# Optimization experiments

Hardware: AMD Instinct MI355X
Metric: run time of the kernel (lower is better)

The kernel has to match this reference:

```python
import jax, jax.numpy as jnp
import numpy as np

N_NODES = 50000
N_EDGES = 400000
IN_DIM = 128
HIDDEN = 128
OUT_DIM = 128
MIX = 4

def _gelu(x):
    return jax.nn.gelu(x, approximate=False)  # torch default erf-GELU

def setup_inputs() -> dict:
    key = jax.random.key(0)
    ks = jax.random.split(key, 8)
    X = jax.random.normal(ks[0], (N_NODES, IN_DIM), dtype=jnp.float32)
    edge_index = jax.random.randint(ks[1], (2, N_EDGES), 0, N_NODES, dtype=jnp.int64)
    s = lambda fan_in: 1.0 / np.sqrt(fan_in)
    W1 = jax.random.uniform(ks[2], (HIDDEN, IN_DIM), jnp.float32, -s(IN_DIM), s(IN_DIM))
    b1 = jax.random.uniform(ks[3], (HIDDEN,), jnp.float32, -s(IN_DIM), s(IN_DIM))
    WA = jax.random.uniform(ks[4], (HIDDEN, HIDDEN), jnp.float32, -s(HIDDEN), s(HIDDEN))
    WB = jax.random.uniform(ks[5], (MIX, HIDDEN), jnp.float32, -s(HIDDEN), s(HIDDEN))
    W2 = jax.random.uniform(ks[6], (OUT_DIM, 2 * HIDDEN), jnp.float32, -s(2 * HIDDEN), s(2 * HIDDEN))
    b2 = jax.random.uniform(ks[7], (OUT_DIM,), jnp.float32, -s(2 * HIDDEN), s(2 * HIDDEN))
    return {"X": X, "edge_index": edge_index, "W1": W1, "b1": b1,
            "WA": WA, "WB": WB, "W2": W2, "b2": b2}

def reference(X, edge_index, W1, b1, WA, WB, W2, b2):
    num_nodes = X.shape[0]
    # ff1 -> gelu (dropout identity in eval)
    H = _gelu(X @ W1.T + b1)                       # (N, h)
    src, dst = edge_index[0], edge_index[1]
    X_src = H[src]                                 # (E, h) gather
    # hyper target weights per edge
    W_tar = _gelu(X_src @ WA.T) @ WB.T             # (E, m)
    # per-edge outer product, scatter_add over dst
    cross = X_src[:, :, None] * W_tar[:, None, :]  # (E, h, m)
    agg = jax.ops.segment_sum(cross, dst, num_segments=num_nodes)  # (N, h, m)
    agg = _gelu(agg)
    # gather back per edge, contract mix dim
    out_edge = jnp.einsum('ehm,em->eh', agg[dst], W_tar)  # (E, h)
    # scatter_mean over dst
    ones = jnp.ones((src.shape[0],), X.dtype)
    cnt = jax.ops.segment_sum(ones, dst, num_segments=num_nodes)   # (N,)
    agg_node = jax.ops.segment_sum(out_edge, dst, num_segments=num_nodes)
    agg_node = agg_node / jnp.maximum(cnt, 1.0)[:, None]           # (N, h)
    # root connection + gelu, ff2
    feat = _gelu(jnp.concatenate([agg_node, H], axis=1))           # (N, 2h)
    out = feat @ W2.T + b2                                          # (N, out)
    return out
```

## Files before the change

### kernel.cpp

```cpp
#include <hip/hip_runtime.h>
#include <hip/hip_bf16.h>

#define NN 50000
#define NE 400000
#define NT 3125

typedef unsigned short u16;
typedef short short8 __attribute__((ext_vector_type(8)));
typedef float f32x4 __attribute__((ext_vector_type(4)));

__device__ __forceinline__ float geluf(float x){ return 0.5f*x*(1.0f+erff(x*0.70710678118654752440f)); }
__device__ __forceinline__ u16 f2bfb(float f){
  union { __hip_bfloat16 h; u16 u; } cv; cv.h = __float2bfloat16(f); return cv.u;
}
__device__ __forceinline__ float bfb2f(u16 u){ return __uint_as_float(((unsigned)u)<<16); }

__global__ __launch_bounds__(256) void k_pre(const float* __restrict__ W1,
    const float* __restrict__ WA, const float* __restrict__ W2,
    u16* __restrict__ W1b, u16* __restrict__ WAb, u16* __restrict__ W2b,
    const int* __restrict__ dst, int* __restrict__ deg)
{
  if (blockIdx.x < 64){
    int i4 = (blockIdx.x*256 + threadIdx.x) * 4;
    const float* srcp; u16* dstp; int off;
    if (i4 < 16384){ srcp = W1; dstp = W1b; off = i4; }
    else if (i4 < 32768){ srcp = WA; dstp = WAb; off = i4 - 16384; }
    else { srcp = W2; dstp = W2b; off = i4 - 32768; }
    float4 v = *(const float4*)(srcp + off);
    ushort4 o;
    o.x = f2bfb(v.x); o.y = f2bfb(v.y); o.z = f2bfb(v.z); o.w = f2bfb(v.w);
    *(ushort4*)(dstp + off) = o;
  } else {
    int e = (blockIdx.x - 64)*256 + threadIdx.x;
    if (e < NE) atomicAdd(&deg[dst[e]], 1);
  }
}

__global__ __launch_bounds__(512) void k_ff1n(const float* __restrict__ X,
    const u16* __restrict__ W1b, const float* __restrict__ b1,
    const u16* __restrict__ WAb, const float* __restrict__ WB,
    u16* __restrict__ Hb, float* __restrict__ T)
{
  extern __shared__ u16 smem[];
  u16* w1s = smem;
  u16* was = smem + 17408;
  const int LDW = 136;
  for (int idx8 = threadIdx.x*8; idx8 < 128*128; idx8 += 512*8){
    int c = idx8 >> 7, k = idx8 & 127;
    *(short8*)&w1s[c*LDW + k] = *(const short8*)(W1b + idx8);
    *(short8*)&was[c*LDW + k] = *(const short8*)(WAb + idx8);
  }
  __syncthreads();
  const int lane = threadIdx.x & 63;
  const int wave = threadIdx.x >> 6;
  const int lrow = lane & 15;
  const int kgrp = lane >> 4;
  u16* hls = smem + 34816 + wave*(16*LDW);
  float4 b1v[8];
  #pragma unroll
  for (int nb = 0; nb < 8; nb++) b1v[nb] = *(const float4*)(b1 + nb*16 + kgrp*4);
  float wbv[4][8];
  #pragma unroll
  for (int m = 0; m < 4; m++)
    #pragma unroll
    for (int nb = 0; nb < 8; nb++)
      wbv[m][nb] = WB[m*128 + nb*16 + lrow];
  for (int tile = blockIdx.x*8 + wave; tile < NT; tile += gridDim.x*8){
    const float* xr = X + (size_t)(tile*16 + lrow)*128 + kgrp*8;
    f32x4 acc[8];
    #pragma unroll
    for (int nb = 0; nb < 8; nb++) acc[nb] = (f32x4){0.f,0.f,0.f,0.f};
    #pragma unroll
    for (int kk = 0; kk < 4; kk++){
      float4 xa = *(const float4*)(xr + kk*32);
      float4 xb = *(const float4*)(xr + kk*32 + 4);
      union { short8 v; u16 u[8]; } af;
      af.u[0]=f2bfb(xa.x); af.u[1]=f2bfb(xa.y); af.u[2]=f2bfb(xa.z); af.u[3]=f2bfb(xa.w);
      af.u[4]=f2bfb(xb.x); af.u[5]=f2bfb(xb.y); af.u[6]=f2bfb(xb.z); af.u[7]=f2bfb(xb.w);
      #pragma unroll
      for (int nb = 0; nb < 8; nb++){
        short8 bf = *(const short8*)&w1s[(nb*16 + lrow)*LDW + kk*32 + kgrp*8];
        acc[nb] = __builtin_amdgcn_mfma_f32_16x16x32_bf16(bf, af.v, acc[nb], 0, 0, 0);
      }
    }
    const size_t rb = (size_t)(tile*16 + lrow)*128 + kgrp*4;
    #pragma unroll
    for (int nb = 0; nb < 8; nb++){
      ushort4 hp;
      #pragma unroll
      for (int r = 0; r < 4; r++)
        ((u16*)&hp)[r] = f2bfb(geluf(acc[nb][r] + b1v[nb][r]));
      *(ushort4*)(Hb + rb + nb*16) = hp;
      *(ushort4*)&hls[lrow*LDW + nb*16 + kgrp*4] = hp;
    }
    f32x4 acc2[8];
    #pragma unroll
    for (int nb = 0; nb < 8; nb++) acc2[nb] = (f32x4){0.f,0.f,0.f,0.f};
    #pragma unroll
    for (int kk = 0; kk < 4; kk++){
      short8 af = *(const short8*)&hls[lrow*LDW + kk*32 + kgrp*8];
      #pragma unroll
      for (int nb = 0; nb < 8; nb++){
        short8 bf = *(const short8*)&was[(nb*16 + lrow)*LDW + kk*32 + kgrp*8];
        acc2[nb] = __builtin_amdgcn_mfma_f32_16x16x32_bf16(af, bf, acc2[nb], 0, 0, 0);
      }
    }
    float part[4][4];
    #pragma unroll
    for (int r = 0; r < 4; r++)
      #pragma unroll
      for (int m = 0; m < 4; m++) part[r][m] = 0.f;
    #pragma unroll
    for (int nb = 0; nb < 8; nb++){
      float g0 = geluf(acc2[nb][0]), g1 = geluf(acc2[nb][1]);
      float g2 = geluf(acc2[nb][2]), g3 = geluf(acc2[nb][3]);
      #pragma unroll
      for (int m = 0; m < 4; m++){
        float w = wbv[m][nb];
        part[0][m] += g0*w; part[1][m] += g1*w;
        part[2][m] += g2*w; part[3][m] += g3*w;
      }
    }
    #pragma unroll
    for (int s = 1; s < 16; s <<= 1)
      #pragma unroll
      for (int r = 0; r < 4; r++)
        #pragma unroll
        for (int m = 0; m < 4; m++)
          part[r][m] += __shfl_xor(part[r][m], s, 64);
    if (lrow == 0){
      #pragma unroll
      for (int r = 0; r < 4; r++){
        f32x4 tv = { part[r][0], part[r][1], part[r][2], part[r][3] };
        *(f32x4*)&T[(size_t)(tile*16 + kgrp*4 + r)*4] = tv;
      }
    }
  }
}

__global__ __launch_bounds__(1024) void k_scan(const int* __restrict__ deg, int* __restrict__ offs){
  __shared__ int wsum[16];
  __shared__ int sbase_s;
  const int tid = threadIdx.x, lane = tid & 63, wave = tid >> 6;
  if (tid == 0) sbase_s = 0;
  __syncthreads();
  for (int base = 0; base < NN; base += 4096){
    int i0 = base + tid*4;
    int v0=0,v1=0,v2=0,v3=0;
    if (i0+3 < NN){ int4 v = *(const int4*)(deg+i0); v0=v.x;v1=v.y;v2=v.z;v3=v.w; }
    else {
      if (i0   < NN) v0 = deg[i0];
      if (i0+1 < NN) v1 = deg[i0+1];
      if (i0+2 < NN) v2 = deg[i0+2];
    }
    int own = v0+v1+v2+v3;
    int inc = own;
    #pragma unroll
    for (int s=1;s<64;s<<=1){ int t = __shfl_up(inc, s, 64); if (lane >= s) inc += t; }
    if (lane == 63) wsum[wave] = inc;
    __syncthreads();
    if (wave == 0 && lane < 16){
      int w = wsum[lane];
      #pragma unroll
      for (int s=1;s<16;s<<=1){ int t = __shfl_up(w, s, 64); if (lane >= s) w += t; }
      wsum[lane] = w;
    }
    __syncthreads();
    int sbase = sbase_s;
    int wbase = sbase + (wave ? wsum[wave-1] : 0);
    int excl = wbase + inc - own;
    if (i0   < NN) offs[i0]   = excl;
    if (i0+1 < NN) offs[i0+1] = excl + v0;
    if (i0+2 < NN) offs[i0+2] = excl + v0+v1;
    if (i0+3 < NN) offs[i0+3] = excl + v0+v1+v2;
    __syncthreads();
    if (tid == 0) sbase_s = sbase + wsum[15];
    __syncthreads();
  }
  if (tid == 0) offs[NN] = sbase_s;
}

__global__ void k_fill(const int* __restrict__ src, const int* __restrict__ dst,
                       const int* __restrict__ offs, int* __restrict__ cur,
                       int* __restrict__ slist){
  int e = blockIdx.x*256 + threadIdx.x;
  if (e < NE){
    int d = dst[e];
    int p = atomicAdd(&cur[d], 1);
    slist[offs[d] + p] = src[e];
  }
}

__global__ __launch_bounds__(256) void k_agg(const u16* __restrict__ Hb,
    const float* __restrict__ T, const int* __restrict__ offs,
    const int* __restrict__ slist, u16* __restrict__ GAb)
{
  const int lane = threadIdx.x & 63;
  const int wave = threadIdx.x >> 6;
  const int vo = lane*2;
  for (int v = blockIdx.x*4 + wave; v < NN; v += gridDim.x*4){
    const int e0 = __builtin_amdgcn_readfirstlane(offs[v]);
    const int e1 = __builtin_amdgcn_readfirstlane(offs[v+1]);
    float ax0=0, ax1=0, ax2=0, ax3=0;
    float ay0=0, ay1=0, ay2=0, ay3=0;
    float s0=0, s1=0, s2=0, s3=0;
    int idx = e0;
    for (; idx + 8 <= e1; idx += 8){
      unsigned pk[8]; float4 tt[8];
      #pragma unroll
      for (int u = 0; u < 8; u++){
        int sn = slist[idx+u];
        pk[u] = *(const unsigned*)(Hb + (size_t)sn*128 + vo);
        tt[u] = *(const float4*)(T + (size_t)sn*4);
      }
      #pragma unroll
      for (int u = 0; u < 8; u++){
        float hx = bfb2f((u16)(pk[u] & 0xffffu));
        float hy = bfb2f((u16)(pk[u] >> 16));
        ax0 += hx*tt[u].x; ax1 += hx*tt[u].y; ax2 += hx*tt[u].z; ax3 += hx*tt[u].w;
        ay0 += hy*tt[u].x; ay1 += hy*tt[u].y; ay2 += hy*tt[u].z; ay3 += hy*tt[u].w;
        s0 += tt[u].x; s1 += tt[u].y; s2 += tt[u].z; s3 += tt[u].w;
      }
    }
    for (; idx + 4 <= e1; idx += 4){
      unsigned pk[4]; float4 tt[4];
      #pragma unroll
      for (int u = 0; u < 4; u++){
        int sn = slist[idx+u];
        pk[u] = *(const unsigned*)(Hb + (size_t)sn*128 + vo);
        tt[u] = *(const float4*)(T + (size_t)sn*4);
      }
      #pragma unroll
      for (int u = 0; u < 4; u++){
        float hx = bfb2f((u16)(pk[u] & 0xffffu));
        float hy = bfb2f((u16)(pk[u] >> 16));
        ax0 += hx*tt[u].x; ax1 += hx*tt[u].y; ax2 += hx*tt[u].z; ax3 += hx*tt[u].w;
        ay0 += hy*tt[u].x; ay1 += hy*tt[u].y; ay2 += hy*tt[u].z; ay3 += hy*tt[u].w;
        s0 += tt[u].x; s1 += tt[u].y; s2 += tt[u].z; s3 += tt[u].w;
      }
    }
    for (; idx < e1; idx++){
      int sn = slist[idx];
      unsigned pk = *(const unsigned*)(Hb + (size_t)sn*128 + vo);
      float hx = bfb2f((u16)(pk & 0xffffu));
      float hy = bfb2f((u16)(pk >> 16));
      float4 wt = *(const float4*)(T + (size_t)sn*4);
      ax0 += hx*wt.x; ax1 += hx*wt.y; ax2 += hx*wt.z; ax3 += hx*wt.w;
      ay0 += hy*wt.x; ay1 += hy*wt.y; ay2 += hy*wt.z; ay3 += hy*wt.w;
      s0 += wt.x; s1 += wt.y; s2 += wt.z; s3 += wt.w;
    }
    float inv = 1.0f / fmaxf((float)(e1 - e0), 1.0f);
    float ox = geluf(ax0)*s0 + geluf(ax1)*s1 + geluf(ax2)*s2 + geluf(ax3)*s3;
    float oy = geluf(ay0)*s0 + geluf(ay1)*s1 + geluf(ay2)*s2 + geluf(ay3)*s3;
    ushort2 res;
    res.x = f2bfb(geluf(ox * inv));
    res.y = f2bfb(geluf(oy * inv));
    *(ushort2*)(GAb + (size_t)v*128 + vo) = res;
  }
}

__global__ __launch_bounds__(512) void k_ff2(const u16* __restrict__ GAb,
    const u16* __restrict__ Hb, const u16* __restrict__ W2b,
    const float* __restrict__ b2, float* __restrict__ out)
{
  extern __shared__ u16 w2s[];
  const int LDW = 264;
  for (int idx8 = threadIdx.x*8; idx8 < 128*256; idx8 += 512*8){
    int o = idx8 >> 8, k = idx8 & 255;
    *(short8*)&w2s[o*LDW + k] = *(const short8*)(W2b + idx8);
  }
  __syncthreads();
  const int lane = threadIdx.x & 63;
  const int wave = threadIdx.x >> 6;
  const int lrow = lane & 15;
  const int kgrp = lane >> 4;
  float4 b2v[8];
  #pragma unroll
  for (int nb = 0; nb < 8; nb++) b2v[nb] = *(const float4*)(b2 + nb*16 + kgrp*4);
  for (int tile = blockIdx.x*8 + wave; tile < NT; tile += gridDim.x*8){
    const int row = tile*16 + lrow;
    const u16* aga = GAb + (size_t)row*128 + kgrp*8;
    const u16* agh = Hb  + (size_t)row*128 + kgrp*8;
    f32x4 acc[8];
    #pragma unroll
    for (int nb = 0; nb < 8; nb++) acc[nb] = (f32x4){0.f,0.f,0.f,0.f};
    #pragma unroll
    for (int kk = 0; kk < 8; kk++){
      short8 af;
      if (kk < 4){
        af = *(const short8*)(aga + kk*32);
      } else {
        short8 hb = *(const short8*)(agh + (kk-4)*32);
        union { short8 v; u16 u[8]; } g;
        #pragma unroll
        for (int j = 0; j < 8; j++)
          g.u[j] = f2bfb(geluf(bfb2f(((const u16*)&hb)[j])));
        af = g.v;
      }
      #pragma unroll
      for (int nb = 0; nb < 8; nb++){
        short8 bf = *(const short8*)&w2s[(nb*16 + lrow)*LDW + kk*32 + kgrp*8];
        acc[nb] = __builtin_amdgcn_mfma_f32_16x16x32_bf16(bf, af, acc[nb], 0, 0, 0);
      }
    }
    float* orp = out + (size_t)row*128 + kgrp*4;
    #pragma unroll
    for (int nb = 0; nb < 8; nb++){
      f32x4 o;
      o[0] = acc[nb][0] + b2v[nb].x;
      o[1] = acc[nb][1] + b2v[nb].y;
      o[2] = acc[nb][2] + b2v[nb].z;
      o[3] = acc[nb][3] + b2v[nb].w;
      *(f32x4*)(orp + nb*16) = o;
    }
  }
}

extern "C" void kernel_launch(void* const* d_in, const int* in_sizes, int n_in,
                              void* d_out, int out_size, void* d_ws, size_t ws_size,
                              hipStream_t stream)
{
  (void)in_sizes; (void)n_in; (void)out_size; (void)ws_size;
  const float* X  = (const float*)d_in[0];
  const int*   ei = (const int*)d_in[1];
  const float* W1 = (const float*)d_in[2];
  const float* b1 = (const float*)d_in[3];
  const float* WA = (const float*)d_in[4];
  const float* WB = (const float*)d_in[5];
  const float* W2 = (const float*)d_in[6];
  const float* b2 = (const float*)d_in[7];
  float* out = (float*)d_out;
  const int* src = ei;
  const int* dst = ei + NE;

  char* p = (char*)d_ws;
  u16*   Hb   = (u16*)(p);
  u16*   GAb  = (u16*)(p + 12800000);
  float* T    = (float*)(p + 25600000);
  int*   deg  = (int*)(p + 26400000);
  int*   cur  = (int*)(p + 26600192);
  int*   offs = (int*)(p + 26800384);
  int*   slist= (int*)(p + 27000832);
  u16*   W1b  = (u16*)(p + 28600832);
  u16*   WAb  = (u16*)(p + 28633600);
  u16*   W2b  = (u16*)(p + 28666368);

  (void)hipMemsetAsync(deg, 0, 400384, stream);

  (void)hipFuncSetAttribute((const void*)k_ff1n, hipFuncAttributeMaxDynamicSharedMemorySize, 104448);
  (void)hipFuncSetAttribute((const void*)k_ff2,  hipFuncAttributeMaxDynamicSharedMemorySize, 128*264*2);

  k_pre <<<64 + (NE+255)/256, 256, 0, stream>>>(W1, WA, W2, W1b, WAb, W2b, dst, deg);
  k_ff1n<<<391, 512, 104448, stream>>>(X, W1b, b1, WAb, WB, Hb, T);
  k_scan<<<1, 1024, 0, stream>>>(deg, offs);
  k_fill<<<(NE+255)/256, 256, 0, stream>>>(src, dst, offs, cur, slist);
  k_agg <<<2048, 256, 0, stream>>>(Hb, T, offs, slist, GAb);
  k_ff2 <<<391, 512, 128*264*2, stream>>>(GAb, Hb, W2b, b2, out);
}
```

Baseline: 166.3 us.

## Drop LDS staging of W2 in ff2 and process two row tiles per wave

k_ff2 no longer copies the 64KB bf16 W2 into shared memory before each block's work. Weights are now read straight from global memory (served by L1/L2), and each wave computes two 16-row tiles so every weight fragment feeds two MFMAs. This removes the per-block LDS fill and its barrier and lifts the LDS limit on occupancy. In exchange it adds global-load latency on the MFMA inner loop and holds more registers for two sets of A fragments and accumulators. The grid is 391 blocks of 256 threads, with each wave taking exactly one pair of tiles instead of looping.

```diff
diff --git a/kernel.cpp b/kernel.cpp
--- a/kernel.cpp
+++ b/kernel.cpp
@@ -259,17 +259,10 @@
   }
 }
 
-__global__ __launch_bounds__(512) void k_ff2(const u16* __restrict__ GAb,
+__global__ __launch_bounds__(256) void k_ff2(const u16* __restrict__ GAb,
     const u16* __restrict__ Hb, const u16* __restrict__ W2b,
     const float* __restrict__ b2, float* __restrict__ out)
 {
-  extern __shared__ u16 w2s[];
-  const int LDW = 264;
-  for (int idx8 = threadIdx.x*8; idx8 < 128*256; idx8 += 512*8){
-    int o = idx8 >> 8, k = idx8 & 255;
-    *(short8*)&w2s[o*LDW + k] = *(const short8*)(W2b + idx8);
-  }
-  __syncthreads();
   const int lane = threadIdx.x & 63;
   const int wave = threadIdx.x >> 6;
   const int lrow = lane & 15;
@@ -277,41 +270,74 @@
   float4 b2v[8];
   #pragma unroll
   for (int nb = 0; nb < 8; nb++) b2v[nb] = *(const float4*)(b2 + nb*16 + kgrp*4);
-  for (int tile = blockIdx.x*8 + wave; tile < NT; tile += gridDim.x*8){
-    const int row = tile*16 + lrow;
-    const u16* aga = GAb + (size_t)row*128 + kgrp*8;
-    const u16* agh = Hb  + (size_t)row*128 + kgrp*8;
-    f32x4 acc[8];
-    #pragma unroll
-    for (int nb = 0; nb < 8; nb++) acc[nb] = (f32x4){0.f,0.f,0.f,0.f};
-    #pragma unroll
-    for (int kk = 0; kk < 8; kk++){
-      short8 af;
-      if (kk < 4){
-        af = *(const short8*)(aga + kk*32);
-      } else {
-        short8 hb = *(const short8*)(agh + (kk-4)*32);
-        union { short8 v; u16 u[8]; } g;
-        #pragma unroll
-        for (int j = 0; j < 8; j++)
-          g.u[j] = f2bfb(geluf(bfb2f(((const u16*)&hb)[j])));
-        af = g.v;
-      }
-      #pragma unroll
-      for (int nb = 0; nb < 8; nb++){
-        short8 bf = *(const short8*)&w2s[(nb*16 + lrow)*LDW + kk*32 + kgrp*8];
-        acc[nb] = __builtin_amdgcn_mfma_f32_16x16x32_bf16(bf, af, acc[nb], 0, 0, 0);
-      }
-    }
-    float* orp = out + (size_t)row*128 + kgrp*4;
+  const int pairIdx = blockIdx.x*4 + wave;
+  const int t0 = pairIdx*2;
+  if (t0 >= NT) return;
+  const int t1 = (t0 + 1 < NT) ? t0 + 1 : t0;
+  const bool do2 = (t0 + 1 < NT);
+
+  const int row0 = t0*16 + lrow;
+  const int row1 = t1*16 + lrow;
+  short8 a0[8], a1[8];
+  {
+    const u16* ga0 = GAb + (size_t)row0*128 + kgrp*8;
+    const u16* hb0 = Hb  + (size_t)row0*128 + kgrp*8;
+    const u16* ga1 = GAb + (size_t)row1*128 + kgrp*8;
+    const u16* hb1 = Hb  + (size_t)row1*128 + kgrp*8;
+    #pragma unroll
+    for (int kk = 0; kk < 4; kk++){
+      a0[kk]   = *(const short8*)(ga0 + kk*32);
+      a1[kk]   = *(const short8*)(ga1 + kk*32);
+      a0[4+kk] = *(const short8*)(hb0 + kk*32);
+      a1[4+kk] = *(const short8*)(hb1 + kk*32);
+    }
+    #pragma unroll
+    for (int kk = 4; kk < 8; kk++){
+      union { short8 v; u16 u[8]; } g0, g1;
+      #pragma unroll
+      for (int j = 0; j < 8; j++){
+        g0.u[j] = f2bfb(geluf(bfb2f(((const u16*)&a0[kk])[j])));
+        g1.u[j] = f2bfb(geluf(bfb2f(((const u16*)&a1[kk])[j])));
+      }
+      a0[kk] = g0.v; a1[kk] = g1.v;
+    }
+  }
+  f32x4 acc0[8], acc1[8];
+  #pragma unroll
+  for (int nb = 0; nb < 8; nb++){
+    acc0[nb] = (f32x4){0.f,0.f,0.f,0.f};
+    acc1[nb] = (f32x4){0.f,0.f,0.f,0.f};
+  }
+  const u16* wrow = W2b + (size_t)lrow*256 + kgrp*8;
+  #pragma unroll
+  for (int kk = 0; kk < 8; kk++){
+    #pragma unroll
+    for (int nb = 0; nb < 8; nb++){
+      short8 bf = *(const short8*)(wrow + (size_t)nb*16*256 + kk*32);
+      acc0[nb] = __builtin_amdgcn_mfma_f32_16x16x32_bf16(bf, a0[kk], acc0[nb], 0, 0, 0);
+      acc1[nb] = __builtin_amdgcn_mfma_f32_16x16x32_bf16(bf, a1[kk], acc1[nb], 0, 0, 0);
+    }
+  }
+  float* or0 = out + (size_t)row0*128 + kgrp*4;
+  #pragma unroll
+  for (int nb = 0; nb < 8; nb++){
+    f32x4 o;
+    o[0] = acc0[nb][0] + b2v[nb].x;
+    o[1] = acc0[nb][1] + b2v[nb].y;
+    o[2] = acc0[nb][2] + b2v[nb].z;
+    o[3] = acc0[nb][3] + b2v[nb].w;
+    *(f32x4*)(or0 + nb*16) = o;
+  }
+  if (do2){
+    float* or1 = out + (size_t)row1*128 + kgrp*4;
     #pragma unroll
     for (int nb = 0; nb < 8; nb++){
       f32x4 o;
-      o[0] = acc[nb][0] + b2v[nb].x;
-      o[1] = acc[nb][1] + b2v[nb].y;
-      o[2] = acc[nb][2] + b2v[nb].z;
-      o[3] = acc[nb][3] + b2v[nb].w;
-      *(f32x4*)(orp + nb*16) = o;
+      o[0] = acc1[nb][0] + b2v[nb].x;
+      o[1] = acc1[nb][1] + b2v[nb].y;
+      o[2] = acc1[nb][2] + b2v[nb].z;
+      o[3] = acc1[nb][3] + b2v[nb].w;
+      *(f32x4*)(or1 + nb*16) = o;
     }
   }
 }
@@ -348,12 +374,11 @@
   (void)hipMemsetAsync(deg, 0, 400384, stream);
 
   (void)hipFuncSetAttribute((const void*)k_ff1n, hipFuncAttributeMaxDynamicSharedMemorySize, 104448);
-  (void)hipFuncSetAttribute((const void*)k_ff2,  hipFuncAttributeMaxDynamicSharedMemorySize, 128*264*2);
 
   k_pre <<<64 + (NE+255)/256, 256, 0, stream>>>(W1, WA, W2, W1b, WAb, W2b, dst, deg);
   k_ff1n<<<391, 512, 104448, stream>>>(X, W1b, b1, WAb, WB, Hb, T);
   k_scan<<<1, 1024, 0, stream>>>(deg, offs);
   k_fill<<<(NE+255)/256, 256, 0, stream>>>(src, dst, offs, cur, slist);
   k_agg <<<2048, 256, 0, stream>>>(Hb, T, offs, slist, GAb);
-  k_ff2 <<<391, 512, 128*264*2, stream>>>(GAb, Hb, W2b, b2, out);
-}
+  k_ff2 <<<391, 256, 0, stream>>>(GAb, Hb, W2b, b2, out);
+}
```

New measurement: 157.8 us. -5.1%, faster.

## Drop LDS staging of W2 in ff2 and use one tile per wave

Applied to the files above, without the earlier changes.

The ff2 kernel no longer copies W2 into shared memory behind a block-wide barrier. It reads W2 fragments directly from global memory, relying on L1/L2 caching of the 64KB bf16 matrix. The launch becomes one 16-row tile per wave across 782 blocks of 256 threads, and each wave preloads all A fragments with GELU applied up front. This removes the per-block LDS fill and sync and frees LDS for occupancy, but it puts more pressure on the L1/L2 path for the weights and adds register pressure from holding eight A fragments.

```diff
diff --git a/kernel.cpp b/kernel.cpp
--- a/kernel.cpp
+++ b/kernel.cpp
@@ -259,60 +259,57 @@
   }
 }
 
-__global__ __launch_bounds__(512) void k_ff2(const u16* __restrict__ GAb,
+__global__ __launch_bounds__(256, 2) void k_ff2(const u16* __restrict__ GAb,
     const u16* __restrict__ Hb, const u16* __restrict__ W2b,
     const float* __restrict__ b2, float* __restrict__ out)
 {
-  extern __shared__ u16 w2s[];
-  const int LDW = 264;
-  for (int idx8 = threadIdx.x*8; idx8 < 128*256; idx8 += 512*8){
-    int o = idx8 >> 8, k = idx8 & 255;
-    *(short8*)&w2s[o*LDW + k] = *(const short8*)(W2b + idx8);
-  }
-  __syncthreads();
   const int lane = threadIdx.x & 63;
   const int wave = threadIdx.x >> 6;
   const int lrow = lane & 15;
   const int kgrp = lane >> 4;
-  float4 b2v[8];
-  #pragma unroll
-  for (int nb = 0; nb < 8; nb++) b2v[nb] = *(const float4*)(b2 + nb*16 + kgrp*4);
-  for (int tile = blockIdx.x*8 + wave; tile < NT; tile += gridDim.x*8){
-    const int row = tile*16 + lrow;
-    const u16* aga = GAb + (size_t)row*128 + kgrp*8;
-    const u16* agh = Hb  + (size_t)row*128 + kgrp*8;
-    f32x4 acc[8];
-    #pragma unroll
-    for (int nb = 0; nb < 8; nb++) acc[nb] = (f32x4){0.f,0.f,0.f,0.f};
-    #pragma unroll
-    for (int kk = 0; kk < 8; kk++){
-      short8 af;
-      if (kk < 4){
-        af = *(const short8*)(aga + kk*32);
-      } else {
-        short8 hb = *(const short8*)(agh + (kk-4)*32);
-        union { short8 v; u16 u[8]; } g;
-        #pragma unroll
-        for (int j = 0; j < 8; j++)
-          g.u[j] = f2bfb(geluf(bfb2f(((const u16*)&hb)[j])));
-        af = g.v;
-      }
-      #pragma unroll
-      for (int nb = 0; nb < 8; nb++){
-        short8 bf = *(const short8*)&w2s[(nb*16 + lrow)*LDW + kk*32 + kgrp*8];
-        acc[nb] = __builtin_amdgcn_mfma_f32_16x16x32_bf16(bf, af, acc[nb], 0, 0, 0);
-      }
-    }
-    float* orp = out + (size_t)row*128 + kgrp*4;
+  const int tile = blockIdx.x*4 + wave;
+  if (tile >= NT) return;
+  const int row = tile*16 + lrow;
+  short8 a[8];
+  {
+    const u16* ga = GAb + (size_t)row*128 + kgrp*8;
+    const u16* hb = Hb  + (size_t)row*128 + kgrp*8;
+    #pragma unroll
+    for (int kk = 0; kk < 4; kk++){
+      a[kk]   = *(const short8*)(ga + kk*32);
+      a[4+kk] = *(const short8*)(hb + kk*32);
+    }
+    #pragma unroll
+    for (int kk = 4; kk < 8; kk++){
+      union { short8 v; u16 u[8]; } g;
+      #pragma unroll
+      for (int j = 0; j < 8; j++)
+        g.u[j] = f2bfb(geluf(bfb2f(((const u16*)&a[kk])[j])));
+      a[kk] = g.v;
+    }
+  }
+  f32x4 acc[8];
+  #pragma unroll
+  for (int nb = 0; nb < 8; nb++) acc[nb] = (f32x4){0.f,0.f,0.f,0.f};
+  const u16* wrow = W2b + (size_t)lrow*256 + kgrp*8;
+  #pragma unroll
+  for (int kk = 0; kk < 8; kk++){
     #pragma unroll
     for (int nb = 0; nb < 8; nb++){
-      f32x4 o;
-      o[0] = acc[nb][0] + b2v[nb].x;
-      o[1] = acc[nb][1] + b2v[nb].y;
-      o[2] = acc[nb][2] + b2v[nb].z;
-      o[3] = acc[nb][3] + b2v[nb].w;
-      *(f32x4*)(orp + nb*16) = o;
-    }
+      short8 bf = *(const short8*)(wrow + (size_t)nb*16*256 + kk*32);
+      acc[nb] = __builtin_amdgcn_mfma_f32_16x16x32_bf16(bf, a[kk], acc[nb], 0, 0, 0);
+    }
+  }
+  float* orp = out + (size_t)row*128 + kgrp*4;
+  #pragma unroll
+  for (int nb = 0; nb < 8; nb++){
+    float4 bv = *(const float4*)(b2 + nb*16 + kgrp*4);
+    f32x4 o;
+    o[0] = acc[nb][0] + bv.x;
+    o[1] = acc[nb][1] + bv.y;
+    o[2] = acc[nb][2] + bv.z;
+    o[3] = acc[nb][3] + bv.w;
+    *(f32x4*)(orp + nb*16) = o;
   }
 }
 
@@ -348,12 +345,11 @@
   (void)hipMemsetAsync(deg, 0, 400384, stream);
 
   (void)hipFuncSetAttribute((const void*)k_ff1n, hipFuncAttributeMaxDynamicSharedMemorySize, 104448);
-  (void)hipFuncSetAttribute((const void*)k_ff2,  hipFuncAttributeMaxDynamicSharedMemorySize, 128*264*2);
 
   k_pre <<<64 + (NE+255)/256, 256, 0, stream>>>(W1, WA, W2, W1b, WAb, W2b, dst, deg);
   k_ff1n<<<391, 512, 104448, stream>>>(X, W1b, b1, WAb, WB, Hb, T);
   k_scan<<<1, 1024, 0, stream>>>(deg, offs);
   k_fill<<<(NE+255)/256, 256, 0, stream>>>(src, dst, offs, cur, slist);
   k_agg <<<2048, 256, 0, stream>>>(Hb, T, offs, slist, GAb);
-  k_ff2 <<<391, 512, 128*264*2, stream>>>(GAb, Hb, W2b, b2, out);
-}
+  k_ff2 <<<(NT+3)/4, 256, 0, stream>>>(GAb, Hb, W2b, b2, out);
+}
```

New measurement: 156.8 us. 1.06x faster.
